# Kernel tuning notes

Measured on AMD Instinct MI355X. Metric: run time of the kernel, lower is better.

Reference implementation:

```python
import jax, jax.numpy as jnp
import numpy as np

E = 16          # num_local_experts
K = 4           # experts_per_token
H = 2048        # hidden_size
I = 2048        # intermediate_size
LIMIT = 7.0     # swiglu_limit
ALPHA = 1.702   # glu_alpha


def setup_inputs() -> dict:
    key = jax.random.key(0)
    ks = jax.random.split(key, 9)
    int8 = lambda k, shp: jax.random.randint(k, shp, -127, 128).astype(jnp.float32)
    return {
        "hidden_states": jax.random.normal(ks[0], (1024, H), dtype=jnp.float32),
        "router_logits": jax.random.normal(ks[1], (1024, E), dtype=jnp.float32),
        "gate_up_proj": int8(ks[2], (E, H, 2 * I)),                      # int8 values in f32
        "gate_up_proj_scale": jax.random.uniform(ks[3], (E, 2 * I), minval=0.5, maxval=1.5) * 0.002,
        "gate_up_proj_bias": jax.random.normal(ks[4], (E, 2 * I), dtype=jnp.float32) * 0.01,
        "gate_up_smooth_scale": jnp.ones((E, I), dtype=jnp.float32),
        "down_proj": int8(ks[5], (E, I, H)),
        "down_proj_scale": jax.random.uniform(ks[6], (E, H), minval=0.5, maxval=1.5) * 0.002,
        "down_proj_bias": jax.random.normal(ks[7], (E, H), dtype=jnp.float32) * 0.01,
    }


def _dyn_quant(x):
    # per-token symmetric int8 dynamic quant (npu_dynamic_quant)
    scale = jnp.maximum(jnp.max(jnp.abs(x), axis=-1, keepdims=True) / 127.0, 1e-8)
    q = jnp.clip(jnp.round(x / scale), -127.0, 127.0)
    return q, scale


def reference(hidden_states, router_logits, gate_up_proj, gate_up_proj_scale,
              gate_up_proj_bias, gate_up_smooth_scale, down_proj,
              down_proj_scale, down_proj_bias):
    T = hidden_states.shape[0]
    C = (2 * T * K) // E

    # --- gating (npu_moe_gating_top_k: softmax + top-k, then renormalize) ---
    probs = jax.nn.softmax(router_logits, axis=-1)
    topk_w, topk_i = jax.lax.top_k(probs, K)                 # [T,K]
    topk_w = topk_w / jnp.sum(topk_w, axis=-1, keepdims=True)

    # --- per-token dynamic quant ---
    x_q, x_scale = _dyn_quant(hidden_states)                 # [T,H], [T,1]

    # --- dispatch (npu_moe_init_routing_v2): token-major expansion, capacity buckets ---
    flat_e = topk_i.reshape(-1)                              # [T*K] expert id per row
    flat_w = topk_w.reshape(-1)                              # [T*K]
    src = jnp.arange(T * K) // K                             # [T*K] source token
    onehot = jax.nn.one_hot(flat_e, E, dtype=jnp.int32)      # [T*K,E]
    pos = jnp.sum(jnp.cumsum(onehot, axis=0) * onehot, axis=1) - 1  # position within expert
    valid = pos < C
    slot = flat_e * C + jnp.where(valid, pos, 0)             # unique for valid rows
    vf = valid.astype(x_q.dtype)[:, None]
    x_disp = jnp.zeros((E * C, H), x_q.dtype).at[slot].add(x_q[src] * vf)
    s_disp = jnp.zeros((E * C, 1), x_scale.dtype).at[slot].add(x_scale[src] * vf)
    x_disp = x_disp.reshape(E, C, H)
    s_disp = s_disp.reshape(E, C, 1)

    gu_i32 = jnp.einsum('ech,ehf->ecf', x_disp, gate_up_proj)          # [E,C,2I]
    y = gu_i32 * s_disp * gate_up_proj_scale[:, None, :] + gate_up_proj_bias[:, None, :]

    # --- gpt-oss swiglu (activate_left, clamp_limit, alpha=1.702, glu_bias=1.0) ---
    gate = jnp.minimum(y[..., :I], LIMIT)
    up = jnp.clip(y[..., I:], -LIMIT, LIMIT)
    act = gate * jax.nn.sigmoid(ALPHA * gate) * (up + 1.0)
    act = act * gate_up_smooth_scale[:, None, :]

    # --- requant + grouped GEMM 2 + dequant ---
    h_q, h_scale = _dyn_quant(act)                                     # [E,C,I], [E,C,1]
    z_i32 = jnp.einsum('eci,eih->ech', h_q, down_proj)                 # [E,C,H]
    z = z_i32 * h_scale * down_proj_scale[:, None, :] + down_proj_bias[:, None, :]

    # --- combine (npu_moe_finalize_routing): weighted scatter-add per source token ---
    gathered = z.reshape(E * C, H)[slot]                               # [T*K,H]
    out = jnp.zeros((T, H), z.dtype).at[src].add(flat_w[:, None] * vf * gathered)
    return out
```

## Files before the change

### kernel.cpp

```cpp
#include <hip/hip_runtime.h>
#include <stdint.h>
#include <stddef.h>

#define T_TOK 1024
#define NE    16
#define TOPK  4
#define HID   2048
#define INTER 2048
#define CAP   512
#define GLIMIT 7.0f
#define GALPHA 1.702f

#define BM  128
#define BK  64

typedef __attribute__((ext_vector_type(4))) int   iv4;
typedef __attribute__((ext_vector_type(4))) float f32x4;

typedef const __attribute__((address_space(1))) unsigned gl_u32;
typedef __attribute__((address_space(3))) unsigned lds_u32;
__device__ __forceinline__ void gl_lds16(const void* g, void* l) {
    __builtin_amdgcn_global_load_lds((gl_u32*)g, (lds_u32*)l, 16, 0, 0);
}

__global__ __launch_bounds__(256) void gating_kernel(
    const float* __restrict__ logits, int* __restrict__ topki, float* __restrict__ topkw)
{
    int t = blockIdx.x * 256 + threadIdx.x;
    if (t >= T_TOK) return;
    float l[NE];
#pragma unroll
    for (int e = 0; e < NE; e++) l[e] = logits[t * NE + e];
    unsigned used = 0;
    float val[TOPK]; int idx[TOPK];
#pragma unroll
    for (int k = 0; k < TOPK; k++) {
        float bv = -3.4e38f; int bi = 0;
#pragma unroll
        for (int e = 0; e < NE; e++) {
            bool ok = (((used >> e) & 1u) == 0u) && (l[e] > bv);
            bv = ok ? l[e] : bv;
            bi = ok ? e : bi;
        }
        used |= (1u << bi); idx[k] = bi; val[k] = bv;
    }
    float m = val[0];
    float s = 0.f, w[TOPK];
#pragma unroll
    for (int k = 0; k < TOPK; k++) { w[k] = expf(val[k] - m); s += w[k]; }
    float inv = 1.0f / s;
#pragma unroll
    for (int k = 0; k < TOPK; k++) { topki[t * TOPK + k] = idx[k]; topkw[t * TOPK + k] = w[k] * inv; }
}

__global__ __launch_bounds__(256) void quant_x_kernel(
    const float* __restrict__ x, char* __restrict__ xq, float* __restrict__ xs)
{
    int t = blockIdx.x;
    const float4* row = (const float4*)(x + (size_t)t * HID);
    __shared__ float red[256];
    float amax = 0.f;
    float4 v0 = row[threadIdx.x];
    float4 v1 = row[threadIdx.x + 256];
    amax = fmaxf(amax, fmaxf(fmaxf(fabsf(v0.x), fabsf(v0.y)), fmaxf(fabsf(v0.z), fabsf(v0.w))));
    amax = fmaxf(amax, fmaxf(fmaxf(fabsf(v1.x), fabsf(v1.y)), fmaxf(fabsf(v1.z), fabsf(v1.w))));
    red[threadIdx.x] = amax; __syncthreads();
    for (int s = 128; s > 0; s >>= 1) {
        if (threadIdx.x < s) red[threadIdx.x] = fmaxf(red[threadIdx.x], red[threadIdx.x + s]);
        __syncthreads();
    }
    float scale = fmaxf(red[0] / 127.0f, 1e-8f);
    if (threadIdx.x == 0) xs[t] = scale;
    char4* orow = (char4*)(xq + (size_t)t * HID);
    {
        char4 c;
        c.x = (char)fminf(fmaxf(rintf(v0.x / scale), -127.f), 127.f);
        c.y = (char)fminf(fmaxf(rintf(v0.y / scale), -127.f), 127.f);
        c.z = (char)fminf(fmaxf(rintf(v0.z / scale), -127.f), 127.f);
        c.w = (char)fminf(fmaxf(rintf(v0.w / scale), -127.f), 127.f);
        orow[threadIdx.x] = c;
        c.x = (char)fminf(fmaxf(rintf(v1.x / scale), -127.f), 127.f);
        c.y = (char)fminf(fmaxf(rintf(v1.y / scale), -127.f), 127.f);
        c.z = (char)fminf(fmaxf(rintf(v1.z / scale), -127.f), 127.f);
        c.w = (char)fminf(fmaxf(rintf(v1.w / scale), -127.f), 127.f);
        orow[threadIdx.x + 256] = c;
    }
}

__global__ __launch_bounds__(1024) void routing_kernel(
    const int* __restrict__ topki, const float* __restrict__ topkw,
    int* __restrict__ row_src, float* __restrict__ row_w, int* __restrict__ counts)
{
    int wv = threadIdx.x >> 6;
    int lane = threadIdx.x & 63;
    int base = 0;
    for (int r0 = 0; r0 < T_TOK * TOPK; r0 += 64) {
        int r = r0 + lane;
        int e = topki[r];
        unsigned long long mask = __ballot(e == wv);
        int pre = __popcll(mask & ((1ULL << lane) - 1ULL));
        if (e == wv) {
            int pos = base + pre;
            if (pos < CAP) {
                row_src[wv * CAP + pos] = r >> 2;
                row_w[wv * CAP + pos] = topkw[r];
            }
        }
        base += __popcll(mask);
    }
    if (lane == 0) counts[wv] = (base < CAP) ? base : CAP;
}

__global__ __launch_bounds__(128) void convw_kernel(
    const float* __restrict__ src, char* __restrict__ dst, int pitch, int mode)
{
    int nt = blockIdx.x, kt = blockIdx.y, e = blockIdx.z;
    int l = threadIdx.x;
    int col;
    if (mode == 0) col = (l < 64) ? (nt * 64 + l) : (INTER + nt * 64 + (l - 64));
    else           col = nt * 128 + l;
    const float* s = src + (size_t)e * 2048 * pitch + (size_t)(kt * 64) * pitch + col;
    int wv[16];
#pragma unroll
    for (int j = 0; j < 16; j++) {
        int v = 0;
#pragma unroll
        for (int bq = 0; bq < 4; bq++) {
            int q = (int)s[(size_t)(j * 4 + bq) * pitch];
            v |= (q & 0xff) << (8 * bq);
        }
        wv[j] = v;
    }
    int4* d = (int4*)(dst + (((size_t)e * gridDim.x + nt) * 32 + kt) * 8192 + l * 64);
#pragma unroll
    for (int j = 0; j < 4; j++)
        d[j] = make_int4(wv[4 * j], wv[4 * j + 1], wv[4 * j + 2], wv[4 * j + 3]);
}

__global__ __launch_bounds__(256) void gemm1_kernel(
    const char* __restrict__ xq, const float* __restrict__ xs,
    const int* __restrict__ row_src, const int* __restrict__ counts,
    const char* __restrict__ gpack, const float* __restrict__ gus,
    const float* __restrict__ gub, const float* __restrict__ smo,
    float* __restrict__ act)
{
    int nt = blockIdx.x;
    int mt = blockIdx.y;
    int e  = blockIdx.z;
    int count = counts[e];
    int m0 = mt * BM;
    if (m0 >= count) return;

    __shared__ char sA[BM * BK];
    __shared__ char sB[128 * BK];

    int t = threadIdx.x;
    int lane = t & 63, w = t >> 6;
    int n16 = lane & 15, quad = lane >> 4;

    const char* aSrc[2];
#pragma unroll
    for (int op = 0; op < 2; op++) {
        int c = op * 256 + t;
        int row = c >> 2, ks = c & 3;
        int gr = m0 + row;
        if (gr > count - 1) gr = count - 1;
        aSrc[op] = xq + (size_t)row_src[e * CAP + gr] * HID + ks * 16;
    }
    const char* bSrc = gpack + (((size_t)e * 32 + nt) * 32) * 8192 + t * 16;

    iv4 acc[2][8];
#pragma unroll
    for (int i = 0; i < 2; i++)
#pragma unroll
        for (int j = 0; j < 8; j++) acc[i][j] = (iv4)0;

    for (int kt = 0; kt < HID / BK; kt++) {
        __syncthreads();
#pragma unroll
        for (int op = 0; op < 2; op++)
            gl_lds16(aSrc[op] + kt * BK, sA + op * 4096 + w * 1024);
#pragma unroll
        for (int op = 0; op < 2; op++)
            gl_lds16(bSrc + kt * 8192 + op * 4096, sB + op * 4096 + w * 1024);
        __syncthreads();

        iv4 af[2], bf[8];
#pragma unroll
        for (int mf = 0; mf < 2; mf++)
            af[mf] = *(const iv4*)(sA + (w * 32 + mf * 16 + n16) * 64 + quad * 16);
#pragma unroll
        for (int nf = 0; nf < 8; nf++)
            bf[nf] = *(const iv4*)(sB + (nf * 16 + n16) * 64 + quad * 16);
#pragma unroll
        for (int mf = 0; mf < 2; mf++)
#pragma unroll
            for (int nf = 0; nf < 8; nf++)
                acc[mf][nf] = __builtin_amdgcn_mfma_i32_16x16x64_i8(af[mf], bf[nf], acc[mf][nf], 0, 0, 0);
    }

    const float* gsc = gus + (size_t)e * (2 * INTER);
    const float* gbi = gub + (size_t)e * (2 * INTER);
    const float* sms = smo + (size_t)e * INTER;
#pragma unroll
    for (int mf = 0; mf < 2; mf++) {
#pragma unroll
        for (int r = 0; r < 4; r++) {
            int gr = m0 + w * 32 + mf * 16 + quad * 4 + r;
            if (gr >= count) continue;
            float srow = xs[row_src[e * CAP + gr]];
            float* arow = act + (size_t)(e * CAP + gr) * INTER;
#pragma unroll
            for (int g = 0; g < 4; g++) {
                int col = nt * 64 + g * 16 + n16;
                float yg = (float)acc[mf][g][r]     * srow * gsc[col]         + gbi[col];
                float yu = (float)acc[mf][g + 4][r] * srow * gsc[INTER + col] + gbi[INTER + col];
                float gate = fminf(yg, GLIMIT);
                float up   = fminf(fmaxf(yu, -GLIMIT), GLIMIT);
                float sig  = 1.0f / (1.0f + expf(-GALPHA * gate));
                arow[col] = gate * sig * (up + 1.0f) * sms[col];
            }
        }
    }
}

__global__ __launch_bounds__(256) void requant_kernel(
    const float* __restrict__ act, const int* __restrict__ counts,
    char* __restrict__ hq, float* __restrict__ hs)
{
    int b = blockIdx.x;
    int e = b >> 9, c = b & (CAP - 1);
    if (c >= counts[e]) return;
    const float4* row = (const float4*)(act + (size_t)b * INTER);
    __shared__ float red[256];
    float4 v0 = row[threadIdx.x];
    float4 v1 = row[threadIdx.x + 256];
    float amax = fmaxf(fmaxf(fabsf(v0.x), fabsf(v0.y)), fmaxf(fabsf(v0.z), fabsf(v0.w)));
    amax = fmaxf(amax, fmaxf(fmaxf(fabsf(v1.x), fabsf(v1.y)), fmaxf(fabsf(v1.z), fabsf(v1.w))));
    red[threadIdx.x] = amax; __syncthreads();
    for (int s = 128; s > 0; s >>= 1) {
        if (threadIdx.x < s) red[threadIdx.x] = fmaxf(red[threadIdx.x], red[threadIdx.x + s]);
        __syncthreads();
    }
    float scale = fmaxf(red[0] / 127.0f, 1e-8f);
    if (threadIdx.x == 0) hs[b] = scale;
    char4* orow = (char4*)(hq + (size_t)b * INTER);
    {
        char4 cc;
        cc.x = (char)fminf(fmaxf(rintf(v0.x / scale), -127.f), 127.f);
        cc.y = (char)fminf(fmaxf(rintf(v0.y / scale), -127.f), 127.f);
        cc.z = (char)fminf(fmaxf(rintf(v0.z / scale), -127.f), 127.f);
        cc.w = (char)fminf(fmaxf(rintf(v0.w / scale), -127.f), 127.f);
        orow[threadIdx.x] = cc;
        cc.x = (char)fminf(fmaxf(rintf(v1.x / scale), -127.f), 127.f);
        cc.y = (char)fminf(fmaxf(rintf(v1.y / scale), -127.f), 127.f);
        cc.z = (char)fminf(fmaxf(rintf(v1.z / scale), -127.f), 127.f);
        cc.w = (char)fminf(fmaxf(rintf(v1.w / scale), -127.f), 127.f);
        orow[threadIdx.x + 256] = cc;
    }
}

__global__ __launch_bounds__(256) void gemm2_kernel(
    const char* __restrict__ hq, const float* __restrict__ hs,
    const int* __restrict__ row_src, const float* __restrict__ row_w,
    const int* __restrict__ counts, const char* __restrict__ dpack,
    const float* __restrict__ dsc, const float* __restrict__ dbi,
    float* __restrict__ out)
{
    int nt = blockIdx.x;
    int mt = blockIdx.y;
    int e  = blockIdx.z;
    int count = counts[e];
    int m0 = mt * BM;
    if (m0 >= count) return;

    __shared__ char sA[BM * BK];
    __shared__ char sB[128 * BK];

    int t = threadIdx.x;
    int lane = t & 63, w = t >> 6;
    int n16 = lane & 15, quad = lane >> 4;

    const char* aSrc[2];
#pragma unroll
    for (int op = 0; op < 2; op++) {
        int c = op * 256 + t;
        int row = c >> 2, ks = c & 3;
        int gr = m0 + row;
        if (gr > count - 1) gr = count - 1;
        aSrc[op] = hq + (size_t)(e * CAP + gr) * INTER + ks * 16;
    }
    const char* bSrc = dpack + (((size_t)e * 16 + nt) * 32) * 8192 + t * 16;

    iv4 acc[2][8];
#pragma unroll
    for (int i = 0; i < 2; i++)
#pragma unroll
        for (int j = 0; j < 8; j++) acc[i][j] = (iv4)0;

    for (int kt = 0; kt < INTER / BK; kt++) {
        __syncthreads();
#pragma unroll
        for (int op = 0; op < 2; op++)
            gl_lds16(aSrc[op] + kt * BK, sA + op * 4096 + w * 1024);
#pragma unroll
        for (int op = 0; op < 2; op++)
            gl_lds16(bSrc + kt * 8192 + op * 4096, sB + op * 4096 + w * 1024);
        __syncthreads();

        iv4 af[2], bf[8];
#pragma unroll
        for (int mf = 0; mf < 2; mf++)
            af[mf] = *(const iv4*)(sA + (w * 32 + mf * 16 + n16) * 64 + quad * 16);
#pragma unroll
        for (int nf = 0; nf < 8; nf++)
            bf[nf] = *(const iv4*)(sB + (nf * 16 + n16) * 64 + quad * 16);
#pragma unroll
        for (int mf = 0; mf < 2; mf++)
#pragma unroll
            for (int nf = 0; nf < 8; nf++)
                acc[mf][nf] = __builtin_amdgcn_mfma_i32_16x16x64_i8(af[mf], bf[nf], acc[mf][nf], 0, 0, 0);
    }

    const float* dscE = dsc + (size_t)e * HID;
    const float* dbiE = dbi + (size_t)e * HID;
#pragma unroll
    for (int mf = 0; mf < 2; mf++) {
#pragma unroll
        for (int r = 0; r < 4; r++) {
            int gr = m0 + w * 32 + mf * 16 + quad * 4 + r;
            if (gr >= count) continue;
            int ri = e * CAP + gr;
            float hsr = hs[ri];
            float wr  = row_w[ri];
            float* orow = out + (size_t)row_src[ri] * HID;
#pragma unroll
            for (int nf = 0; nf < 8; nf++) {
                int col = nt * 128 + nf * 16 + n16;
                float z = (float)acc[mf][nf][r] * hsr * dscE[col] + dbiE[col];
                atomicAdd(&orow[col], wr * z);
            }
        }
    }
}

extern "C" void kernel_launch(void* const* d_in, const int* in_sizes, int n_in,
                              void* d_out, int out_size, void* d_ws, size_t ws_size,
                              hipStream_t stream)
{
    (void)in_sizes; (void)n_in; (void)out_size; (void)ws_size;
    const float* x   = (const float*)d_in[0];
    const float* rl  = (const float*)d_in[1];
    const float* gup = (const float*)d_in[2];
    const float* gus = (const float*)d_in[3];
    const float* gub = (const float*)d_in[4];
    const float* smo = (const float*)d_in[5];
    const float* dwn = (const float*)d_in[6];
    const float* dsc = (const float*)d_in[7];
    const float* dbi = (const float*)d_in[8];
    float* out = (float*)d_out;

    char* p = (char*)d_ws;
    auto carve = [&](size_t bytes) -> char* {
        char* r = p; p += (bytes + 255) & ~(size_t)255; return r;
    };
    char* xq       = carve((size_t)T_TOK * HID);
    float* xs      = (float*)carve((size_t)T_TOK * 4);
    int* topki     = (int*)carve((size_t)T_TOK * TOPK * 4);
    float* topkw   = (float*)carve((size_t)T_TOK * TOPK * 4);
    int* counts    = (int*)carve((size_t)NE * 4);
    int* rsrc      = (int*)carve((size_t)NE * CAP * 4);
    float* rw      = (float*)carve((size_t)NE * CAP * 4);
    float* actb    = (float*)carve((size_t)NE * CAP * INTER * 4);
    char* hq       = carve((size_t)NE * CAP * INTER);
    float* hsb     = (float*)carve((size_t)NE * CAP * 4);
    char* gpack    = carve((size_t)NE * 32 * 32 * 8192);
    char* dpack    = carve((size_t)NE * 16 * 32 * 8192);

    hipMemsetAsync(d_out, 0, (size_t)T_TOK * HID * 4, stream);
    gating_kernel<<<dim3((T_TOK + 255) / 256), 256, 0, stream>>>(rl, topki, topkw);
    quant_x_kernel<<<dim3(T_TOK), 256, 0, stream>>>(x, xq, xs);
    routing_kernel<<<dim3(1), 1024, 0, stream>>>(topki, topkw, rsrc, rw, counts);
    convw_kernel<<<dim3(32, 32, NE), 128, 0, stream>>>(gup, gpack, 2 * INTER, 0);
    convw_kernel<<<dim3(16, 32, NE), 128, 0, stream>>>(dwn, dpack, HID, 1);
    gemm1_kernel<<<dim3(INTER / 64, CAP / BM, NE), 256, 0, stream>>>(
        xq, xs, rsrc, counts, gpack, gus, gub, smo, actb);
    requant_kernel<<<dim3(NE * CAP), 256, 0, stream>>>(actb, counts, hq, hsb);
    gemm2_kernel<<<dim3(HID / 128, CAP / BM, NE), 256, 0, stream>>>(
        hq, hsb, rsrc, rw, counts, dpack, dsc, dbi, out);
}
```

Before: 1.094 ms.

## Fuse f32-to-int8 weight conversion into GEMM B-tile loads with swizzled LDS

Removes the separate convw passes that pack the f32 weights into an int8 tile layout. Each GEMM block now reads its f32 weight columns directly, converts them to int8 in registers and writes them to LDS. An XOR swizzle on both the A and B LDS layouts is added to reduce bank conflicts. The trade-off is that every M-tile re-reads the full f32 weights (up to 4 M-tiles per expert), using strided column loads with no overlap against the MFMA work. This may cost more than the one-time conversion it replaces.

Result: slower. 1.180 ms (+7.9%).

```diff
diff --git a/kernel.cpp b/kernel.cpp
--- a/kernel.cpp
+++ b/kernel.cpp
@@ -15,12 +15,16 @@
 #define BK  64
 
 typedef __attribute__((ext_vector_type(4))) int   iv4;
-typedef __attribute__((ext_vector_type(4))) float f32x4;
 
 typedef const __attribute__((address_space(1))) unsigned gl_u32;
 typedef __attribute__((address_space(3))) unsigned lds_u32;
 __device__ __forceinline__ void gl_lds16(const void* g, void* l) {
     __builtin_amdgcn_global_load_lds((gl_u32*)g, (lds_u32*)l, 16, 0, 0);
+}
+
+__device__ __forceinline__ int pack4(float a, float b, float c, float d) {
+    int qa = (int)a, qb = (int)b, qc = (int)c, qd = (int)d;
+    return (qa & 255) | ((qb & 255) << 8) | ((qc & 255) << 16) | (qd << 24);
 }
 
 __global__ __launch_bounds__(256) void gating_kernel(
@@ -59,10 +63,9 @@
     int t = blockIdx.x;
     const float4* row = (const float4*)(x + (size_t)t * HID);
     __shared__ float red[256];
-    float amax = 0.f;
     float4 v0 = row[threadIdx.x];
     float4 v1 = row[threadIdx.x + 256];
-    amax = fmaxf(amax, fmaxf(fmaxf(fabsf(v0.x), fabsf(v0.y)), fmaxf(fabsf(v0.z), fabsf(v0.w))));
+    float amax = fmaxf(fmaxf(fabsf(v0.x), fabsf(v0.y)), fmaxf(fabsf(v0.z), fabsf(v0.w)));
     amax = fmaxf(amax, fmaxf(fmaxf(fabsf(v1.x), fabsf(v1.y)), fmaxf(fabsf(v1.z), fabsf(v1.w))));
     red[threadIdx.x] = amax; __syncthreads();
     for (int s = 128; s > 0; s >>= 1) {
@@ -111,36 +114,10 @@
     if (lane == 0) counts[wv] = (base < CAP) ? base : CAP;
 }
 
-__global__ __launch_bounds__(128) void convw_kernel(
-    const float* __restrict__ src, char* __restrict__ dst, int pitch, int mode)
-{
-    int nt = blockIdx.x, kt = blockIdx.y, e = blockIdx.z;
-    int l = threadIdx.x;
-    int col;
-    if (mode == 0) col = (l < 64) ? (nt * 64 + l) : (INTER + nt * 64 + (l - 64));
-    else           col = nt * 128 + l;
-    const float* s = src + (size_t)e * 2048 * pitch + (size_t)(kt * 64) * pitch + col;
-    int wv[16];
-#pragma unroll
-    for (int j = 0; j < 16; j++) {
-        int v = 0;
-#pragma unroll
-        for (int bq = 0; bq < 4; bq++) {
-            int q = (int)s[(size_t)(j * 4 + bq) * pitch];
-            v |= (q & 0xff) << (8 * bq);
-        }
-        wv[j] = v;
-    }
-    int4* d = (int4*)(dst + (((size_t)e * gridDim.x + nt) * 32 + kt) * 8192 + l * 64);
-#pragma unroll
-    for (int j = 0; j < 4; j++)
-        d[j] = make_int4(wv[4 * j], wv[4 * j + 1], wv[4 * j + 2], wv[4 * j + 3]);
-}
-
 __global__ __launch_bounds__(256) void gemm1_kernel(
     const char* __restrict__ xq, const float* __restrict__ xs,
     const int* __restrict__ row_src, const int* __restrict__ counts,
-    const char* __restrict__ gpack, const float* __restrict__ gus,
+    const float* __restrict__ gup, const float* __restrict__ gus,
     const float* __restrict__ gub, const float* __restrict__ smo,
     float* __restrict__ act)
 {
@@ -157,17 +134,26 @@
     int t = threadIdx.x;
     int lane = t & 63, w = t >> 6;
     int n16 = lane & 15, quad = lane >> 4;
+    int swq = quad ^ ((n16 >> 1) & 3);
 
     const char* aSrc[2];
 #pragma unroll
     for (int op = 0; op < 2; op++) {
         int c = op * 256 + t;
         int row = c >> 2, ks = c & 3;
+        int ksg = ks ^ ((row >> 1) & 3);
         int gr = m0 + row;
         if (gr > count - 1) gr = count - 1;
-        aSrc[op] = xq + (size_t)row_src[e * CAP + gr] * HID + ks * 16;
-    }
-    const char* bSrc = gpack + (((size_t)e * 32 + nt) * 32) * 8192 + t * 16;
+        aSrc[op] = xq + (size_t)row_src[e * CAP + gr] * HID + ksg * 16;
+    }
+
+    int bn = t >> 1;
+    int kb = (t & 1) * 32;
+    int colg = nt * 64 + (bn & 63) + ((bn >= 64) ? INTER : 0);
+    const float* bsrc = gup + (size_t)e * HID * (2 * INTER) + colg;
+    int sn = (bn >> 1) & 3;
+    char* wp0 = sB + bn * 64 + (((kb >> 4) + 0) ^ sn) * 16;
+    char* wp1 = sB + bn * 64 + (((kb >> 4) + 1) ^ sn) * 16;
 
     iv4 acc[2][8];
 #pragma unroll
@@ -175,23 +161,29 @@
 #pragma unroll
         for (int j = 0; j < 8; j++) acc[i][j] = (iv4)0;
 
-    for (int kt = 0; kt < HID / BK; kt++) {
-        __syncthreads();
-#pragma unroll
-        for (int op = 0; op < 2; op++)
-            gl_lds16(aSrc[op] + kt * BK, sA + op * 4096 + w * 1024);
-#pragma unroll
-        for (int op = 0; op < 2; op++)
-            gl_lds16(bSrc + kt * 8192 + op * 4096, sB + op * 4096 + w * 1024);
+    for (int k0 = 0; k0 < HID; k0 += BK) {
+        float f[32];
+#pragma unroll
+        for (int i = 0; i < 32; i++)
+            f[i] = bsrc[(size_t)(k0 + kb + i) * (2 * INTER)];
+        __syncthreads();
+        gl_lds16(aSrc[0] + k0, sA + w * 1024);
+        gl_lds16(aSrc[1] + k0, sA + 4096 + w * 1024);
+        int d[8];
+#pragma unroll
+        for (int j = 0; j < 8; j++)
+            d[j] = pack4(f[4 * j], f[4 * j + 1], f[4 * j + 2], f[4 * j + 3]);
+        *(int4*)wp0 = make_int4(d[0], d[1], d[2], d[3]);
+        *(int4*)wp1 = make_int4(d[4], d[5], d[6], d[7]);
         __syncthreads();
 
         iv4 af[2], bf[8];
 #pragma unroll
         for (int mf = 0; mf < 2; mf++)
-            af[mf] = *(const iv4*)(sA + (w * 32 + mf * 16 + n16) * 64 + quad * 16);
+            af[mf] = *(const iv4*)(sA + (w * 32 + mf * 16 + n16) * 64 + swq * 16);
 #pragma unroll
         for (int nf = 0; nf < 8; nf++)
-            bf[nf] = *(const iv4*)(sB + (nf * 16 + n16) * 64 + quad * 16);
+            bf[nf] = *(const iv4*)(sB + (nf * 16 + n16) * 64 + swq * 16);
 #pragma unroll
         for (int mf = 0; mf < 2; mf++)
 #pragma unroll
@@ -263,7 +255,7 @@
 __global__ __launch_bounds__(256) void gemm2_kernel(
     const char* __restrict__ hq, const float* __restrict__ hs,
     const int* __restrict__ row_src, const float* __restrict__ row_w,
-    const int* __restrict__ counts, const char* __restrict__ dpack,
+    const int* __restrict__ counts, const float* __restrict__ dwn,
     const float* __restrict__ dsc, const float* __restrict__ dbi,
     float* __restrict__ out)
 {
@@ -280,17 +272,26 @@
     int t = threadIdx.x;
     int lane = t & 63, w = t >> 6;
     int n16 = lane & 15, quad = lane >> 4;
+    int swq = quad ^ ((n16 >> 1) & 3);
 
     const char* aSrc[2];
 #pragma unroll
     for (int op = 0; op < 2; op++) {
         int c = op * 256 + t;
         int row = c >> 2, ks = c & 3;
+        int ksg = ks ^ ((row >> 1) & 3);
         int gr = m0 + row;
         if (gr > count - 1) gr = count - 1;
-        aSrc[op] = hq + (size_t)(e * CAP + gr) * INTER + ks * 16;
-    }
-    const char* bSrc = dpack + (((size_t)e * 16 + nt) * 32) * 8192 + t * 16;
+        aSrc[op] = hq + (size_t)(e * CAP + gr) * INTER + ksg * 16;
+    }
+
+    int bn = t >> 1;
+    int kb = (t & 1) * 32;
+    int colg = nt * 128 + bn;
+    const float* bsrc = dwn + (size_t)e * INTER * HID + colg;
+    int sn = (bn >> 1) & 3;
+    char* wp0 = sB + bn * 64 + (((kb >> 4) + 0) ^ sn) * 16;
+    char* wp1 = sB + bn * 64 + (((kb >> 4) + 1) ^ sn) * 16;
 
     iv4 acc[2][8];
 #pragma unroll
@@ -298,23 +299,29 @@
 #pragma unroll
         for (int j = 0; j < 8; j++) acc[i][j] = (iv4)0;
 
-    for (int kt = 0; kt < INTER / BK; kt++) {
-        __syncthreads();
-#pragma unroll
-        for (int op = 0; op < 2; op++)
-            gl_lds16(aSrc[op] + kt * BK, sA + op * 4096 + w * 1024);
-#pragma unroll
-        for (int op = 0; op < 2; op++)
-            gl_lds16(bSrc + kt * 8192 + op * 4096, sB + op * 4096 + w * 1024);
+    for (int k0 = 0; k0 < INTER; k0 += BK) {
+        float f[32];
+#pragma unroll
+        for (int i = 0; i < 32; i++)
+            f[i] = bsrc[(size_t)(k0 + kb + i) * HID];
+        __syncthreads();
+        gl_lds16(aSrc[0] + k0, sA + w * 1024);
+        gl_lds16(aSrc[1] + k0, sA + 4096 + w * 1024);
+        int d[8];
+#pragma unroll
+        for (int j = 0; j < 8; j++)
+            d[j] = pack4(f[4 * j], f[4 * j + 1], f[4 * j + 2], f[4 * j + 3]);
+        *(int4*)wp0 = make_int4(d[0], d[1], d[2], d[3]);
+        *(int4*)wp1 = make_int4(d[4], d[5], d[6], d[7]);
         __syncthreads();
 
         iv4 af[2], bf[8];
 #pragma unroll
         for (int mf = 0; mf < 2; mf++)
-            af[mf] = *(const iv4*)(sA + (w * 32 + mf * 16 + n16) * 64 + quad * 16);
+            af[mf] = *(const iv4*)(sA + (w * 32 + mf * 16 + n16) * 64 + swq * 16);
 #pragma unroll
         for (int nf = 0; nf < 8; nf++)
-            bf[nf] = *(const iv4*)(sB + (nf * 16 + n16) * 64 + quad * 16);
+            bf[nf] = *(const iv4*)(sB + (nf * 16 + n16) * 64 + swq * 16);
 #pragma unroll
         for (int mf = 0; mf < 2; mf++)
 #pragma unroll
@@ -374,18 +381,14 @@
     float* actb    = (float*)carve((size_t)NE * CAP * INTER * 4);
     char* hq       = carve((size_t)NE * CAP * INTER);
     float* hsb     = (float*)carve((size_t)NE * CAP * 4);
-    char* gpack    = carve((size_t)NE * 32 * 32 * 8192);
-    char* dpack    = carve((size_t)NE * 16 * 32 * 8192);
 
     hipMemsetAsync(d_out, 0, (size_t)T_TOK * HID * 4, stream);
     gating_kernel<<<dim3((T_TOK + 255) / 256), 256, 0, stream>>>(rl, topki, topkw);
     quant_x_kernel<<<dim3(T_TOK), 256, 0, stream>>>(x, xq, xs);
     routing_kernel<<<dim3(1), 1024, 0, stream>>>(topki, topkw, rsrc, rw, counts);
-    convw_kernel<<<dim3(32, 32, NE), 128, 0, stream>>>(gup, gpack, 2 * INTER, 0);
-    convw_kernel<<<dim3(16, 32, NE), 128, 0, stream>>>(dwn, dpack, HID, 1);
     gemm1_kernel<<<dim3(INTER / 64, CAP / BM, NE), 256, 0, stream>>>(
-        xq, xs, rsrc, counts, gpack, gus, gub, smo, actb);
+        xq, xs, rsrc, counts, gup, gus, gub, smo, actb);
     requant_kernel<<<dim3(NE * CAP), 256, 0, stream>>>(actb, counts, hq, hsb);
     gemm2_kernel<<<dim3(HID / 128, CAP / BM, NE), 256, 0, stream>>>(
-        hq, hsb, rsrc, rw, counts, dpack, dsc, dbi, out);
-}
+        hq, hsb, rsrc, rw, counts, dwn, dsc, dbi, out);
+}
```
